# Performance work log

Measured on AMD Instinct MI355X. Metric: run time of the kernel, lower is better.

Reference implementation:

```python
import jax, jax.numpy as jnp
import numpy as np

NEG_INF = -1.0e9


def setup_inputs() -> dict:
    key = jax.random.key(0)
    ks = jax.random.split(key, 7)
    B, D, L, N, K = 4096, 512, 20, 8192, 64
    return {
        "inputs_embed": jax.random.normal(ks[0], (B, D), jnp.float32),
        "labels_embed": jax.random.normal(ks[1], (B, D), jnp.float32),
        "labels": jax.random.normal(ks[2], (B, L), jnp.float32),
        "all_labels_embed": jax.random.normal(ks[3], (N, D), jnp.float32),
        "all_labels": jax.random.normal(ks[4], (N, L), jnp.float32),
        "neg_ids_in": jax.random.randint(ks[5], (B, K), 0, B, jnp.int32),
        "neg_ids_lb": jax.random.randint(ks[6], (B, K), 0, N, jnp.int32),
    }


def reference(inputs_embed, labels_embed, labels, all_labels_embed, all_labels,
              neg_ids_in, neg_ids_lb):
    # --- negative sampling (indices supplied; equals tf.gather of tiled table) ---
    neg_ie = inputs_embed[neg_ids_in]        # [B,K,D] negatives from inputs
    neg_le = all_labels_embed[neg_ids_lb]    # [B,K,D] negatives from label table
    # bad-negative masks: negative label features identical to the positive's
    bad_in = jnp.all(labels[neg_ids_in] == labels[:, None, :], axis=-1).astype(inputs_embed.dtype)      # [B,K]
    bad_lb = jnp.all(all_labels[neg_ids_lb] == labels[:, None, :], axis=-1).astype(inputs_embed.dtype)  # [B,K]

    # --- similarities (dot products) ---
    sim_pos = jnp.sum(inputs_embed * labels_embed, axis=-1, keepdims=True)            # [B,1]
    sim_neg_il = jnp.einsum("bd,bkd->bk", inputs_embed, neg_le) + NEG_INF * bad_lb    # [B,K]
    sim_neg_ll = jnp.einsum("bd,bkd->bk", labels_embed, neg_le) + NEG_INF * bad_lb
    sim_neg_ii = jnp.einsum("bd,bkd->bk", inputs_embed, neg_ie) + NEG_INF * bad_in
    sim_neg_li = jnp.einsum("bd,bkd->bk", labels_embed, neg_ie) + NEG_INF * bad_in

    # --- accuracy ---
    max_all = jnp.max(jnp.concatenate([sim_pos, sim_neg_il], axis=-1), axis=-1)
    acc = jnp.mean((max_all == sim_pos[:, 0]).astype(jnp.float32))

    # --- softmax loss, correct class at index 0 ---
    logits = jnp.concatenate([sim_pos, sim_neg_il, sim_neg_ll, sim_neg_ii, sim_neg_li], axis=-1)  # [B,1+4K]
    per_ex = -jax.nn.log_softmax(logits, axis=-1)[:, 0]   # [B]

    # --- confidence-based loss scaling: loss_scale(-per_ex) ---
    q = jnp.exp(-per_ex)
    scale = jnp.where(jnp.max(q) > 0.5,
                      jax.lax.stop_gradient(((1.0 - q) / 0.5) ** 4),
                      jnp.ones_like(q))
    loss = jnp.mean(per_ex * scale)
    return loss, acc
```

## Files before the change

kernel.cpp:

```cpp
#include <hip/hip_runtime.h>
#include <hip/hip_bf16.h>

#define BB 4096
#define DD 512
#define LLAB 20
#define NN 8192
#define KK 64

constexpr float kNegInf = -1.0e9f;
constexpr float kLn2 = 0.69314718055994530942f;
constexpr float kWlPe = 2.5f;
constexpr float kWlTie = 2.0f;
constexpr double kFix = 1073741824.0;

#define OFF_PEREX 0
#define OFF_STATS 16384
#define OFF_MINPE (16384 + 256)
#define OFF_SUMP  (16384 + 512)
#define OFF_SUMS  (16384 + 1024)
#define OFF_SP    36864
#define OFF_SIE   53248
#define OFF_SLE   69632
#define OFF_SALE  86016
#define OFF_HLAB  118784
#define OFF_HAL   151552
#define OFF_IEQ   217088
#define OFF_LEQ   (OFF_IEQ + (size_t)BB * DD)
#define OFF_ALEQ  (OFF_LEQ + (size_t)BB * DD)
#define WS_NEED   (OFF_ALEQ + (size_t)NN * DD)

typedef unsigned u32x4 __attribute__((ext_vector_type(4)));

#define GLD(dst, base, OFFSTR)                                        \
  asm volatile("global_load_dwordx4 %0, %1, off offset:" OFFSTR      \
               : "=v"(dst) : "v"(base) : "memory")

__device__ __forceinline__ float dot4(const float4& a, const float4& b) {
  return a.x * b.x + a.y * b.y + a.z * b.z + a.w * b.w;
}

__device__ __forceinline__ float waveReduceSum(float v) {
#pragma unroll
  for (int s = 1; s < 64; s <<= 1) v += __shfl_xor(v, s);
  return v;
}

__device__ __forceinline__ float waveReduceMax(float v) {
#pragma unroll
  for (int s = 1; s < 64; s <<= 1) v = fmaxf(v, __shfl_xor(v, s));
  return v;
}

__device__ __forceinline__ float waveReduceMin(float v) {
#pragma unroll
  for (int s = 1; s < 64; s <<= 1) v = fminf(v, __shfl_xor(v, s));
  return v;
}

__device__ __forceinline__ unsigned long long hash20(const float* __restrict__ p) {
  unsigned long long h = 1469598103934665603ull;
#pragma unroll
  for (int t = 0; t < LLAB; ++t) {
    h ^= (unsigned long long)__float_as_uint(p[t]);
    h *= 1099511628211ull;
  }
  return h;
}

__device__ __forceinline__ int sdot4i(unsigned a, unsigned b, int acc) {
#if __has_builtin(__builtin_amdgcn_sdot4)
  return __builtin_amdgcn_sdot4((int)a, (int)b, acc, false);
#else
#pragma unroll
  for (int t = 0; t < 4; ++t)
    acc += (int)(signed char)(a >> (8 * t)) * (int)(signed char)(b >> (8 * t));
  return acc;
#endif
}

__device__ __forceinline__ unsigned pk4i8(float a, float b, float c, float d, float inv) {
  const int q0 = (int)rintf(a * inv);
  const int q1 = (int)rintf(b * inv);
  const int q2 = (int)rintf(c * inv);
  const int q3 = (int)rintf(d * inv);
  return (q0 & 255) | ((q1 & 255) << 8) | ((q2 & 255) << 16) | ((q3 & 255) << 24);
}

__device__ __forceinline__ float max8abs(const float4& a, const float4& c) {
  return fmaxf(fmaxf(fmaxf(fabsf(a.x), fabsf(a.y)), fmaxf(fabsf(a.z), fabsf(a.w))),
               fmaxf(fmaxf(fabsf(c.x), fabsf(c.y)), fmaxf(fabsf(c.z), fabsf(c.w))));
}

__device__ __forceinline__ float loss_scale(float pe) {
  const float q = expf(-pe);
  const float t = 2.0f * (1.0f - q);
  const float t2 = t * t;
  return t2 * t2;
}

__device__ __forceinline__ void accum_loss(int b, float pe, unsigned* minpeB,
                                           unsigned long long* sumP,
                                           unsigned long long* sumS) {
  const float pc = fmaxf(pe, 0.0f);
  const int bank = b & 63;
  atomicMin(&minpeB[bank], __float_as_uint(pc));
  atomicAdd(&sumP[bank], (unsigned long long)((double)pc * kFix + 0.5));
  atomicAdd(&sumS[bank],
            (unsigned long long)((double)(pc * loss_scale(pc)) * kFix + 0.5));
}

__global__ void init_kernel(unsigned* stats) {
  if (threadIdx.x == 0) stats[0] = 0u;
}

__global__ __launch_bounds__(256) void prep_kernel(
    const float* __restrict__ ie, const float* __restrict__ le,
    const float* __restrict__ ale, const float* __restrict__ labels,
    const float* __restrict__ al, char* __restrict__ ie_q,
    char* __restrict__ le_q, char* __restrict__ ale_q,
    float* __restrict__ s_ie, float* __restrict__ s_le,
    float* __restrict__ s_ale, float* __restrict__ sp,
    unsigned long long* __restrict__ h_lab,
    unsigned long long* __restrict__ h_al, unsigned* __restrict__ stats,
    unsigned* __restrict__ minpeB, unsigned long long* __restrict__ sumP,
    unsigned long long* __restrict__ sumS) {
  const int tid = threadIdx.x;
  const int lane = tid & 63;
  const int wave = tid >> 6;
  const int w = blockIdx.x * 4 + wave;

  if (w < BB) {
    const float4* i4 = (const float4*)(ie + (size_t)w * DD);
    const float4* l4 = (const float4*)(le + (size_t)w * DD);
    const float4 a0 = i4[2 * lane], a1 = i4[2 * lane + 1];
    const float4 b0 = l4[2 * lane], b1 = l4[2 * lane + 1];
    float p = dot4(a0, b0) + dot4(a1, b1);
    p = waveReduceSum(p);
    float mi = fmaxf(waveReduceMax(max8abs(a0, a1)), 1e-20f);
    const float inv_i = 127.0f / mi;
    uint2 oi;
    oi.x = pk4i8(a0.x, a0.y, a0.z, a0.w, inv_i);
    oi.y = pk4i8(a1.x, a1.y, a1.z, a1.w, inv_i);
    ((uint2*)(ie_q + (size_t)w * DD))[lane] = oi;
    float ml = fmaxf(waveReduceMax(max8abs(b0, b1)), 1e-20f);
    const float inv_l = 127.0f / ml;
    uint2 ol;
    ol.x = pk4i8(b0.x, b0.y, b0.z, b0.w, inv_l);
    ol.y = pk4i8(b1.x, b1.y, b1.z, b1.w, inv_l);
    ((uint2*)(le_q + (size_t)w * DD))[lane] = ol;
    if (lane == 0) {
      sp[w] = p;
      s_ie[w] = mi * (1.0f / 127.0f);
      s_le[w] = ml * (1.0f / 127.0f);
    }
  } else {
    const int row = w - BB;
    const float4* r4 = (const float4*)(ale + (size_t)row * DD);
    const float4 a = r4[2 * lane], c = r4[2 * lane + 1];
    float mx = fmaxf(waveReduceMax(max8abs(a, c)), 1e-20f);
    const float inv = 127.0f / mx;
    uint2 o;
    o.x = pk4i8(a.x, a.y, a.z, a.w, inv);
    o.y = pk4i8(c.x, c.y, c.z, c.w, inv);
    ((uint2*)(ale_q + (size_t)row * DD))[lane] = o;
    if (lane == 0) s_ale[row] = mx * (1.0f / 127.0f);
  }

  const int g = blockIdx.x * 256 + tid;
  if (g < 2) stats[g] = 0u;
  if (g < 64) {
    minpeB[g] = 0x7F800000u;
    sumP[g] = 0ull;
    sumS[g] = 0ull;
  }
  if (g < BB) h_lab[g] = hash20(labels + (size_t)g * LLAB);
  else if (g < BB + NN) h_al[g - BB] = hash20(al + (size_t)(g - BB) * LLAB);
}

__device__ __forceinline__ void row_f32_body(
    int b, const float* __restrict__ ie, const float* __restrict__ le,
    const float* __restrict__ labels, const float* __restrict__ ale,
    const float* __restrict__ al, const int* __restrict__ nin,
    const int* __restrict__ nlb, float* __restrict__ per_ex,
    unsigned* __restrict__ stats, bool count_acc, float* sims, float* wred) {
  const int tid = threadIdx.x;
  const int lane = tid & 63;
  const int wave = tid >> 6;

  const float4* ie4 = (const float4*)(ie + (size_t)b * DD);
  const float4* le4 = (const float4*)(le + (size_t)b * DD);
  float4 ier0 = ie4[lane], ier1 = ie4[lane + 64];
  float4 ler0 = le4[lane], ler1 = le4[lane + 64];
  float lab = (lane < LLAB) ? labels[(size_t)b * LLAB + lane] : 0.0f;

  if (wave == 0) {
    float p = dot4(ier0, ler0) + dot4(ier1, ler1);
    p = waveReduceSum(p);
    if (lane == 0) sims[0] = p;
  }

#pragma unroll 2
  for (int kk = 0; kk < KK / 4; ++kk) {
    const int k = wave * (KK / 4) + kk;
    const int j_lb = __builtin_amdgcn_readfirstlane(nlb[(size_t)b * KK + k]);
    const int j_in = __builtin_amdgcn_readfirstlane(nin[(size_t)b * KK + k]);

    const float4* rle = (const float4*)(ale + (size_t)j_lb * DD);
    const float4* rie = (const float4*)(ie + (size_t)j_in * DD);
    float4 vle0 = rle[lane], vle1 = rle[lane + 64];
    float4 vie0 = rie[lane], vie1 = rie[lane + 64];

    bool ein = true, elb = true;
    if (lane < LLAB) {
      ein = (labels[(size_t)j_in * LLAB + lane] == lab);
      elb = (al[(size_t)j_lb * LLAB + lane] == lab);
    }
    const bool bad_in = (__ballot(ein) == ~0ull);
    const bool bad_lb = (__ballot(elb) == ~0ull);

    float a_il = dot4(vle0, ier0) + dot4(vle1, ier1);
    float a_ll = dot4(vle0, ler0) + dot4(vle1, ler1);
    float a_ii = dot4(vie0, ier0) + dot4(vie1, ier1);
    float a_li = dot4(vie0, ler0) + dot4(vie1, ler1);

    const bool oddl = (lane & 1) != 0;
    float sx = oddl ? a_il : a_ii;
    float sy = oddl ? a_ll : a_li;
    float rx = __shfl_xor(sx, 1);
    float ry = __shfl_xor(sy, 1);
    float mx = (oddl ? a_ii : a_il) + rx;
    float my = (oddl ? a_li : a_ll) + ry;
    const bool hi2 = (lane & 2) != 0;
    float s1 = hi2 ? mx : my;
    float r1 = __shfl_xor(s1, 2);
    float v = (hi2 ? my : mx) + r1;
    v += __shfl_xor(v, 4);
    v += __shfl_xor(v, 8);
    v += __shfl_xor(v, 16);
    v += __shfl_xor(v, 32);

    if (lane < 4) {
      const bool badf = (lane & 1) ? bad_in : bad_lb;
      const float s = badf ? v + kNegInf : v;
      const int slot = ((lane & 1) << 1) | ((lane >> 1) & 1);
      sims[1 + slot * KK + k] = s;
    }
  }
  __syncthreads();

  const float v = sims[1 + tid];
  const float s0 = sims[0];
  float wmax = waveReduceMax(v);
  if (lane == 0) wred[wave] = wmax;
  __syncthreads();
  float m = fmaxf(fmaxf(wred[0], wred[1]), fmaxf(wred[2], wred[3]));
  m = fmaxf(m, s0);
  const float e = expf(v - m);
  float wsum = waveReduceSum(e);
  if (lane == 0) wred[4 + wave] = wsum;
  __syncthreads();
  if (tid == 0) {
    const float tot = wred[4] + wred[5] + wred[6] + wred[7] + expf(s0 - m);
    per_ex[b] = m + logf(tot) - s0;
    if (count_acc) {
      const float max_il = wred[0];
      if (s0 >= max_il) atomicAdd(&stats[0], 1u);
    }
  }
}

__global__ __launch_bounds__(256, 4) void row_i8_kernel(
    const float* __restrict__ ie, const float* __restrict__ le,
    const float* __restrict__ labels, const float* __restrict__ ale,
    const float* __restrict__ al, const char* __restrict__ ie_q,
    const char* __restrict__ le_q, const char* __restrict__ ale_q,
    const float* __restrict__ s_ie, const float* __restrict__ s_le,
    const float* __restrict__ s_ale, const float* __restrict__ sp,
    const unsigned long long* __restrict__ h_lab,
    const unsigned long long* __restrict__ h_al,
    const int* __restrict__ nin, const int* __restrict__ nlb,
    float* __restrict__ per_ex, unsigned* __restrict__ stats,
    unsigned* __restrict__ minpeB, unsigned long long* __restrict__ sumP,
    unsigned long long* __restrict__ sumS) {
  const int b = blockIdx.x;
  const int tid = threadIdx.x;
  const int lane = tid & 63;
  const int wave = tid >> 6;
  const int c = lane & 3;
  const int g = lane >> 2;

  __shared__ u32x4 qls4[64];
  __shared__ float simsX[1 + 4 * KK];
  __shared__ float wred[12];
  __shared__ int do_fix;

  {
    const u32x4* qsrc = (lane < 32)
        ? ((const u32x4*)(ie_q + ((size_t)b << 9))) + lane
        : ((const u32x4*)(le_q + ((size_t)b << 9))) + (lane - 32);
    qls4[lane] = *qsrc;
  }

  const int wuni = __builtin_amdgcn_readfirstlane(wave);
  const int k = wuni * 16 + g;
  const int jl = nlb[b * KK + k];
  const int ji = nin[b * KK + k];
  const char* pa = ale_q + ((size_t)jl << 9) + (c << 4);
  const char* pb = ie_q + ((size_t)ji << 9) + (c << 4);

  u32x4 A0, A1, A2, A3, A4, A5, A6, A7;
  u32x4 B0, B1, B2, B3, B4, B5, B6, B7;
  GLD(A0, pa, "0");   GLD(A1, pa, "64");  GLD(A2, pa, "128"); GLD(A3, pa, "192");
  GLD(A4, pa, "256"); GLD(A5, pa, "320"); GLD(A6, pa, "384"); GLD(A7, pa, "448");
  GLD(B0, pb, "0");   GLD(B1, pb, "64");  GLD(B2, pb, "128"); GLD(B3, pb, "192");
  GLD(B4, pb, "256"); GLD(B5, pb, "320"); GLD(B6, pb, "384"); GLD(B7, pb, "448");

  const unsigned long long hb = h_lab[b];
  const bool bad_lb = (h_al[jl] == hb);
  const bool bad_in = (h_lab[ji] == hb);
  const float sA = s_ale[jl];
  const float sB = s_ie[ji];
  const float s0 = sp[b];
  const float sqi = s_ie[b];
  const float sql = s_le[b];

  asm volatile("s_waitcnt vmcnt(0)" ::: "memory");
  __builtin_amdgcn_sched_barrier(0);

  int il = 0, ll = 0, ii = 0, li = 0;
#define STEP(Ai, Bi, i)                                              \
  {                                                                  \
    const u32x4 qi = qls4[(i) * 4 + c];                              \
    const u32x4 ql = qls4[32 + (i) * 4 + c];                         \
    il = sdot4i(Ai.x, qi.x, il); il = sdot4i(Ai.y, qi.y, il);        \
    il = sdot4i(Ai.z, qi.z, il); il = sdot4i(Ai.w, qi.w, il);        \
    ll = sdot4i(Ai.x, ql.x, ll); ll = sdot4i(Ai.y, ql.y, ll);        \
    ll = sdot4i(Ai.z, ql.z, ll); ll = sdot4i(Ai.w, ql.w, ll);        \
    ii = sdot4i(Bi.x, qi.x, ii); ii = sdot4i(Bi.y, qi.y, ii);        \
    ii = sdot4i(Bi.z, qi.z, ii); ii = sdot4i(Bi.w, qi.w, ii);        \
    li = sdot4i(Bi.x, ql.x, li); li = sdot4i(Bi.y, ql.y, li);        \
    li = sdot4i(Bi.z, ql.z, li); li = sdot4i(Bi.w, ql.w, li);        \
  }
  STEP(A0, B0, 0) STEP(A1, B1, 1) STEP(A2, B2, 2) STEP(A3, B3, 3)
  STEP(A4, B4, 4) STEP(A5, B5, 5) STEP(A6, B6, 6) STEP(A7, B7, 7)
#undef STEP

  const bool odd = (lane & 1) != 0;
  const int x = odd ? il : ii;
  const int y = odd ? ll : li;
  const int rx = __shfl_xor(x, 1);
  const int ry = __shfl_xor(y, 1);
  const int aa = (odd ? ii : il) + rx;
  const int bb2 = (odd ? li : ll) + ry;
  const bool hi2 = (lane & 2) != 0;
  const int s1 = hi2 ? aa : bb2;
  const int r1 = __shfl_xor(s1, 2);
  const int vi = (hi2 ? bb2 : aa) + r1;

  const float srow = (c & 1) ? sB : sA;
  const float sq = (c & 2) ? sql : sqi;
  const float v = (float)vi * (srow * sq);
  const bool badf = (c & 1) ? bad_in : bad_lb;
  const float s = badf ? v + kNegInf : v;

  float m_w = waveReduceMax(s);
  float mil_w = waveReduceMax((c == 0) ? s : -3.0e38f);
  if (lane == 0) {
    wred[wave] = m_w;
    wred[4 + wave] = mil_w;
  }
  __syncthreads();
  float m = fmaxf(fmaxf(fmaxf(wred[0], wred[1]), fmaxf(wred[2], wred[3])), s0);
  const float e = expf(s - m);
  float sum_w = waveReduceSum(e);
  if (lane == 0) wred[8 + wave] = sum_w;
  __syncthreads();
  if (tid == 0) {
    const float tot =
        wred[8] + wred[9] + wred[10] + wred[11] + expf(s0 - m);
    const float pe = m + logf(tot) - s0;
    per_ex[b] = pe;
    const float max_il = fmaxf(fmaxf(wred[4], wred[5]), fmaxf(wred[6], wred[7]));
    const bool wl_row = (pe < kWlPe) || (fabsf(s0 - max_il) < kWlTie);
    do_fix = wl_row ? 1 : 0;
    if (!wl_row) {
      if (s0 >= max_il) atomicAdd(&stats[0], 1u);
      accum_loss(b, pe, minpeB, sumP, sumS);
    }
  }
  __syncthreads();

  if (do_fix) {
    row_f32_body(b, ie, le, labels, ale, al, nin, nlb, per_ex, stats,
                 true, simsX, wred);
    if (tid == 0) accum_loss(b, per_ex[b], minpeB, sumP, sumS);
  }
}

__global__ __launch_bounds__(256) void row_f32_kernel(
    const float* __restrict__ ie, const float* __restrict__ le,
    const float* __restrict__ labels, const float* __restrict__ ale,
    const float* __restrict__ al, const int* __restrict__ nin,
    const int* __restrict__ nlb, float* __restrict__ per_ex,
    unsigned* __restrict__ stats) {
  __shared__ float sims[1 + 4 * KK];
  __shared__ float wred[8];
  row_f32_body(blockIdx.x, ie, le, labels, ale, al, nin, nlb, per_ex, stats,
               true, sims, wred);
}

__global__ __launch_bounds__(64) void finalize2_kernel(
    const unsigned* __restrict__ stats, const unsigned* __restrict__ minpeB,
    const unsigned long long* __restrict__ sumP,
    const unsigned long long* __restrict__ sumS, float* __restrict__ out) {
  const int lane = threadIdx.x;
  unsigned mb = minpeB[lane];
  unsigned long long p = sumP[lane];
  unsigned long long q = sumS[lane];
#pragma unroll
  for (int s = 1; s < 64; s <<= 1) {
    mb = min(mb, (unsigned)__shfl_xor((int)mb, s));
    p += (unsigned long long)__shfl_xor((long long)p, s);
    q += (unsigned long long)__shfl_xor((long long)q, s);
  }
  if (lane == 0) {
    const float minpe = __uint_as_float(mb);
    const bool scale_on = (minpe < kLn2);
    const double tot = (double)(scale_on ? q : p) / kFix;
    out[0] = (float)(tot / (double)BB);
    out[1] = (float)stats[0] / (float)BB;
  }
}

__global__ __launch_bounds__(256) void finalize_kernel(
    const float* __restrict__ per_ex, const unsigned* __restrict__ stats,
    float* __restrict__ out) {
  __shared__ float pe_s[BB];
  __shared__ float wred[8];
  const int tid = threadIdx.x;
  const int lane = tid & 63;
  const int wave = tid >> 6;

  float mn = 1.0e30f;
#pragma unroll 4
  for (int i = tid; i < BB; i += 256) {
    const float v = per_ex[i];
    pe_s[i] = v;
    mn = fminf(mn, v);
  }
  mn = waveReduceMin(mn);
  if (lane == 0) wred[wave] = mn;
  __syncthreads();
  const float minpe = fminf(fminf(wred[0], wred[1]), fminf(wred[2], wred[3]));
  const bool scale_on = (minpe < kLn2);
  __syncthreads();

  float sum = 0.0f;
#pragma unroll 4
  for (int i = tid; i < BB; i += 256) {
    const float pe = pe_s[i];
    sum += pe * (scale_on ? loss_scale(pe) : 1.0f);
  }
  sum = waveReduceSum(sum);
  if (lane == 0) wred[4 + wave] = sum;
  __syncthreads();
  if (tid == 0) {
    const float tot = wred[4] + wred[5] + wred[6] + wred[7];
    out[0] = tot / (float)BB;
    out[1] = (float)stats[0] / (float)BB;
  }
}

extern "C" void kernel_launch(void* const* d_in, const int* in_sizes, int n_in,
                              void* d_out, int out_size, void* d_ws, size_t ws_size,
                              hipStream_t stream) {
  const float* ie = (const float*)d_in[0];
  const float* le = (const float*)d_in[1];
  const float* labels = (const float*)d_in[2];
  const float* ale = (const float*)d_in[3];
  const float* al = (const float*)d_in[4];
  const int* nin = (const int*)d_in[5];
  const int* nlb = (const int*)d_in[6];
  float* out = (float*)d_out;

  float* per_ex = (float*)d_ws;
  unsigned* stats = (unsigned*)((char*)d_ws + OFF_STATS);

  if (ws_size >= WS_NEED) {
    char* ie_q = (char*)d_ws + OFF_IEQ;
    char* le_q = (char*)d_ws + OFF_LEQ;
    char* ale_q = (char*)d_ws + OFF_ALEQ;
    float* s_ie = (float*)((char*)d_ws + OFF_SIE);
    float* s_le = (float*)((char*)d_ws + OFF_SLE);
    float* s_ale = (float*)((char*)d_ws + OFF_SALE);
    float* sp = (float*)((char*)d_ws + OFF_SP);
    unsigned long long* h_lab = (unsigned long long*)((char*)d_ws + OFF_HLAB);
    unsigned long long* h_al = (unsigned long long*)((char*)d_ws + OFF_HAL);
    unsigned* minpeB = (unsigned*)((char*)d_ws + OFF_MINPE);
    unsigned long long* sumP = (unsigned long long*)((char*)d_ws + OFF_SUMP);
    unsigned long long* sumS = (unsigned long long*)((char*)d_ws + OFF_SUMS);

    const int prep_blocks = (BB + NN) / 4;
    hipLaunchKernelGGL(prep_kernel, dim3(prep_blocks), dim3(256), 0, stream,
                       ie, le, ale, labels, al, ie_q, le_q, ale_q,
                       s_ie, s_le, s_ale, sp, h_lab, h_al, stats,
                       minpeB, sumP, sumS);
    hipLaunchKernelGGL(row_i8_kernel, dim3(BB), dim3(256), 0, stream,
                       ie, le, labels, ale, al, ie_q, le_q, ale_q,
                       s_ie, s_le, s_ale, sp, h_lab, h_al, nin, nlb,
                       per_ex, stats, minpeB, sumP, sumS);
    hipLaunchKernelGGL(finalize2_kernel, dim3(1), dim3(64), 0, stream,
                       stats, minpeB, sumP, sumS, out);
  } else {
    hipLaunchKernelGGL(init_kernel, dim3(1), dim3(64), 0, stream, stats);
    hipLaunchKernelGGL(row_f32_kernel, dim3(BB), dim3(256), 0, stream,
                       ie, le, labels, ale, al, nin, nlb, per_ex, stats);
    hipLaunchKernelGGL(finalize_kernel, dim3(1), dim3(256), 0, stream,
                       per_ex, stats, out);
  }
}
```

Baseline: 53.63 us.

## Process four rows per block with double-buffered gather loads overlapping compute

The int8 row kernel now handles four batch rows per block, launching a quarter as many blocks. It preloads indices, scales and bad-negative flags into shared memory, with the bad flag encoded as the sign of the scale. Gathered negatives are fetched in two register sets so the loads for the next half-row overlap the dot products of the current one. The aim is to hide gather latency and amortise per-block setup, at the cost of fewer blocks, more registers and serialised per-row softmax barriers.

```diff
diff --git a/kernel.cpp b/kernel.cpp
--- a/kernel.cpp
+++ b/kernel.cpp
@@ -34,6 +34,16 @@
 #define GLD(dst, base, OFFSTR)                                        \
   asm volatile("global_load_dwordx4 %0, %1, off offset:" OFFSTR      \
                : "=v"(dst) : "v"(base) : "memory")
+
+#define VWAIT8 do { asm volatile("s_waitcnt vmcnt(8)" ::: "memory"); \
+                    __builtin_amdgcn_sched_barrier(0); } while (0)
+#define VWAIT0 do { asm volatile("s_waitcnt vmcnt(0)" ::: "memory"); \
+                    __builtin_amdgcn_sched_barrier(0); } while (0)
+
+#define LBAR do { __builtin_amdgcn_sched_barrier(0);                  \
+                  asm volatile("s_waitcnt lgkmcnt(0)" ::: "memory");  \
+                  __builtin_amdgcn_s_barrier();                       \
+                  __builtin_amdgcn_sched_barrier(0); } while (0)
 
 __device__ __forceinline__ float dot4(const float4& a, const float4& b) {
   return a.x * b.x + a.y * b.y + a.z * b.z + a.w * b.w;
@@ -269,7 +279,7 @@
   }
 }
 
-__global__ __launch_bounds__(256, 4) void row_i8_kernel(
+__global__ __launch_bounds__(256) void row_i8_kernel(
     const float* __restrict__ ie, const float* __restrict__ le,
     const float* __restrict__ labels, const float* __restrict__ ale,
     const float* __restrict__ al, const char* __restrict__ ie_q,
@@ -282,119 +292,186 @@
     float* __restrict__ per_ex, unsigned* __restrict__ stats,
     unsigned* __restrict__ minpeB, unsigned long long* __restrict__ sumP,
     unsigned long long* __restrict__ sumS) {
-  const int b = blockIdx.x;
+  const int b0 = blockIdx.x * 4;
   const int tid = threadIdx.x;
   const int lane = tid & 63;
   const int wave = tid >> 6;
-  const int c = lane & 3;
-  const int g = lane >> 2;
-
-  __shared__ u32x4 qls4[64];
-  __shared__ float simsX[1 + 4 * KK];
-  __shared__ float wred[12];
+  const int o = lane & 7;
+  const int oct = lane >> 3;
+
+  __shared__ u32x4 qls[256];
+  __shared__ int jls[256], jis[256];
+  __shared__ float sAs[256], sBs[256];
+  __shared__ float sims[1 + 4 * KK];
+  __shared__ float wred[8];
   __shared__ int do_fix;
 
   {
+    const int r = wave;
+    const int br = b0 + r;
     const u32x4* qsrc = (lane < 32)
-        ? ((const u32x4*)(ie_q + ((size_t)b << 9))) + lane
-        : ((const u32x4*)(le_q + ((size_t)b << 9))) + (lane - 32);
-    qls4[lane] = *qsrc;
-  }
-
-  const int wuni = __builtin_amdgcn_readfirstlane(wave);
-  const int k = wuni * 16 + g;
-  const int jl = nlb[b * KK + k];
-  const int ji = nin[b * KK + k];
-  const char* pa = ale_q + ((size_t)jl << 9) + (c << 4);
-  const char* pb = ie_q + ((size_t)ji << 9) + (c << 4);
+        ? ((const u32x4*)(ie_q + ((size_t)br << 9))) + lane
+        : ((const u32x4*)(le_q + ((size_t)br << 9))) + (lane - 32);
+    qls[r * 64 + lane] = *qsrc;
+
+    const int k = tid & 63;
+    const int jl = nlb[br * KK + k];
+    const int ji = nin[br * KK + k];
+    const unsigned long long hbr = h_lab[br];
+    const bool blb = (h_al[jl] == hbr);
+    const bool bin = (h_lab[ji] == hbr);
+    const float sa = s_ale[jl];
+    const float sb = s_ie[ji];
+    jls[tid] = jl;
+    jis[tid] = ji;
+    sAs[tid] = blb ? -sa : sa;
+    sBs[tid] = bin ? -sb : sb;
+  }
+  float sp_r[4], sqi_r[4], sql_r[4];
+#pragma unroll
+  for (int rr = 0; rr < 4; ++rr) {
+    sp_r[rr] = sp[b0 + rr];
+    sqi_r[rr] = s_ie[b0 + rr];
+    sql_r[rr] = s_le[b0 + rr];
+  }
+  __syncthreads();
 
   u32x4 A0, A1, A2, A3, A4, A5, A6, A7;
   u32x4 B0, B1, B2, B3, B4, B5, B6, B7;
-  GLD(A0, pa, "0");   GLD(A1, pa, "64");  GLD(A2, pa, "128"); GLD(A3, pa, "192");
-  GLD(A4, pa, "256"); GLD(A5, pa, "320"); GLD(A6, pa, "384"); GLD(A7, pa, "448");
-  GLD(B0, pb, "0");   GLD(B1, pb, "64");  GLD(B2, pb, "128"); GLD(B3, pb, "192");
-  GLD(B4, pb, "256"); GLD(B5, pb, "320"); GLD(B6, pb, "384"); GLD(B7, pb, "448");
-
-  const unsigned long long hb = h_lab[b];
-  const bool bad_lb = (h_al[jl] == hb);
-  const bool bad_in = (h_lab[ji] == hb);
-  const float sA = s_ale[jl];
-  const float sB = s_ie[ji];
-  const float s0 = sp[b];
-  const float sqi = s_ie[b];
-  const float sql = s_le[b];
-
-  asm volatile("s_waitcnt vmcnt(0)" ::: "memory");
-  __builtin_amdgcn_sched_barrier(0);
-
-  int il = 0, ll = 0, ii = 0, li = 0;
-#define STEP(Ai, Bi, i)                                              \
-  {                                                                  \
-    const u32x4 qi = qls4[(i) * 4 + c];                              \
-    const u32x4 ql = qls4[32 + (i) * 4 + c];                         \
-    il = sdot4i(Ai.x, qi.x, il); il = sdot4i(Ai.y, qi.y, il);        \
-    il = sdot4i(Ai.z, qi.z, il); il = sdot4i(Ai.w, qi.w, il);        \
-    ll = sdot4i(Ai.x, ql.x, ll); ll = sdot4i(Ai.y, ql.y, ll);        \
-    ll = sdot4i(Ai.z, ql.z, ll); ll = sdot4i(Ai.w, ql.w, ll);        \
-    ii = sdot4i(Bi.x, qi.x, ii); ii = sdot4i(Bi.y, qi.y, ii);        \
-    ii = sdot4i(Bi.z, qi.z, ii); ii = sdot4i(Bi.w, qi.w, ii);        \
-    li = sdot4i(Bi.x, ql.x, li); li = sdot4i(Bi.y, ql.y, li);        \
-    li = sdot4i(Bi.z, ql.z, li); li = sdot4i(Bi.w, ql.w, li);        \
-  }
-  STEP(A0, B0, 0) STEP(A1, B1, 1) STEP(A2, B2, 2) STEP(A3, B3, 3)
-  STEP(A4, B4, 4) STEP(A5, B5, 5) STEP(A6, B6, 6) STEP(A7, B7, 7)
-#undef STEP
-
-  const bool odd = (lane & 1) != 0;
-  const int x = odd ? il : ii;
-  const int y = odd ? ll : li;
-  const int rx = __shfl_xor(x, 1);
-  const int ry = __shfl_xor(y, 1);
-  const int aa = (odd ? ii : il) + rx;
-  const int bb2 = (odd ? li : ll) + ry;
-  const bool hi2 = (lane & 2) != 0;
-  const int s1 = hi2 ? aa : bb2;
-  const int r1 = __shfl_xor(s1, 2);
-  const int vi = (hi2 ? bb2 : aa) + r1;
-
-  const float srow = (c & 1) ? sB : sA;
-  const float sq = (c & 2) ? sql : sqi;
-  const float v = (float)vi * (srow * sq);
-  const bool badf = (c & 1) ? bad_in : bad_lb;
-  const float s = badf ? v + kNegInf : v;
-
-  float m_w = waveReduceMax(s);
-  float mil_w = waveReduceMax((c == 0) ? s : -3.0e38f);
-  if (lane == 0) {
-    wred[wave] = m_w;
-    wred[4 + wave] = mil_w;
-  }
-  __syncthreads();
-  float m = fmaxf(fmaxf(fmaxf(wred[0], wred[1]), fmaxf(wred[2], wred[3])), s0);
-  const float e = expf(s - m);
-  float sum_w = waveReduceSum(e);
-  if (lane == 0) wred[8 + wave] = sum_w;
-  __syncthreads();
-  if (tid == 0) {
-    const float tot =
-        wred[8] + wred[9] + wred[10] + wred[11] + expf(s0 - m);
-    const float pe = m + logf(tot) - s0;
-    per_ex[b] = pe;
-    const float max_il = fmaxf(fmaxf(wred[4], wred[5]), fmaxf(wred[6], wred[7]));
-    const bool wl_row = (pe < kWlPe) || (fabsf(s0 - max_il) < kWlTie);
-    do_fix = wl_row ? 1 : 0;
-    if (!wl_row) {
-      if (s0 >= max_il) atomicAdd(&stats[0], 1u);
-      accum_loss(b, pe, minpeB, sumP, sumS);
-    }
-  }
-  __syncthreads();
-
-  if (do_fix) {
-    row_f32_body(b, ie, le, labels, ale, al, nin, nlb, per_ex, stats,
-                 true, simsX, wred);
-    if (tid == 0) accum_loss(b, per_ex[b], minpeB, sumP, sumS);
-  }
+
+#define ISSUE8(S, rr, hh)                                                 \
+  {                                                                       \
+    const int k_ = (hh) * 32 + (wave << 3) + oct;                         \
+    const int jl_ = jls[(rr) * 64 + k_];                                  \
+    const int ji_ = jis[(rr) * 64 + k_];                                  \
+    const char* pa_ = ale_q + ((size_t)jl_ << 9) + (o << 4);              \
+    const char* pb_ = ie_q + ((size_t)ji_ << 9) + (o << 4);               \
+    GLD(S##0, pa_, "0");   GLD(S##1, pa_, "128");                         \
+    GLD(S##2, pa_, "256"); GLD(S##3, pa_, "384");                         \
+    GLD(S##4, pb_, "0");   GLD(S##5, pb_, "128");                         \
+    GLD(S##6, pb_, "256"); GLD(S##7, pb_, "384");                         \
+  }
+
+#define COMPUTE8(S, rr, hh)                                               \
+  {                                                                       \
+    const u32x4 a0_ = S##0, a1_ = S##1, a2_ = S##2, a3_ = S##3;           \
+    const u32x4 e0_ = S##4, e1_ = S##5, e2_ = S##6, e3_ = S##7;           \
+    const int k_ = (hh) * 32 + (wave << 3) + oct;                         \
+    const u32x4 q0 = qls[(rr) * 64 + o];                                  \
+    const u32x4 q1 = qls[(rr) * 64 + o + 8];                              \
+    const u32x4 q2 = qls[(rr) * 64 + o + 16];                             \
+    const u32x4 q3 = qls[(rr) * 64 + o + 24];                             \
+    const u32x4 l0 = qls[(rr) * 64 + 32 + o];                             \
+    const u32x4 l1 = qls[(rr) * 64 + 32 + o + 8];                         \
+    const u32x4 l2 = qls[(rr) * 64 + 32 + o + 16];                        \
+    const u32x4 l3 = qls[(rr) * 64 + 32 + o + 24];                        \
+    int il = 0, ll = 0, ii = 0, li = 0;                                   \
+    il = sdot4i(a0_.x, q0.x, il); il = sdot4i(a0_.y, q0.y, il);           \
+    il = sdot4i(a0_.z, q0.z, il); il = sdot4i(a0_.w, q0.w, il);           \
+    il = sdot4i(a1_.x, q1.x, il); il = sdot4i(a1_.y, q1.y, il);           \
+    il = sdot4i(a1_.z, q1.z, il); il = sdot4i(a1_.w, q1.w, il);           \
+    il = sdot4i(a2_.x, q2.x, il); il = sdot4i(a2_.y, q2.y, il);           \
+    il = sdot4i(a2_.z, q2.z, il); il = sdot4i(a2_.w, q2.w, il);           \
+    il = sdot4i(a3_.x, q3.x, il); il = sdot4i(a3_.y, q3.y, il);           \
+    il = sdot4i(a3_.z, q3.z, il); il = sdot4i(a3_.w, q3.w, il);           \
+    ll = sdot4i(a0_.x, l0.x, ll); ll = sdot4i(a0_.y, l0.y, ll);           \
+    ll = sdot4i(a0_.z, l0.z, ll); ll = sdot4i(a0_.w, l0.w, ll);           \
+    ll = sdot4i(a1_.x, l1.x, ll); ll = sdot4i(a1_.y, l1.y, ll);           \
+    ll = sdot4i(a1_.z, l1.z, ll); ll = sdot4i(a1_.w, l1.w, ll);           \
+    ll = sdot4i(a2_.x, l2.x, ll); ll = sdot4i(a2_.y, l2.y, ll);           \
+    ll = sdot4i(a2_.z, l2.z, ll); ll = sdot4i(a2_.w, l2.w, ll);           \
+    ll = sdot4i(a3_.x, l3.x, ll); ll = sdot4i(a3_.y, l3.y, ll);           \
+    ll = sdot4i(a3_.z, l3.z, ll); ll = sdot4i(a3_.w, l3.w, ll);           \
+    ii = sdot4i(e0_.x, q0.x, ii); ii = sdot4i(e0_.y, q0.y, ii);           \
+    ii = sdot4i(e0_.z, q0.z, ii); ii = sdot4i(e0_.w, q0.w, ii);           \
+    ii = sdot4i(e1_.x, q1.x, ii); ii = sdot4i(e1_.y, q1.y, ii);           \
+    ii = sdot4i(e1_.z, q1.z, ii); ii = sdot4i(e1_.w, q1.w, ii);           \
+    ii = sdot4i(e2_.x, q2.x, ii); ii = sdot4i(e2_.y, q2.y, ii);           \
+    ii = sdot4i(e2_.z, q2.z, ii); ii = sdot4i(e2_.w, q2.w, ii);           \
+    ii = sdot4i(e3_.x, q3.x, ii); ii = sdot4i(e3_.y, q3.y, ii);           \
+    ii = sdot4i(e3_.z, q3.z, ii); ii = sdot4i(e3_.w, q3.w, ii);           \
+    li = sdot4i(e0_.x, l0.x, li); li = sdot4i(e0_.y, l0.y, li);           \
+    li = sdot4i(e0_.z, l0.z, li); li = sdot4i(e0_.w, l0.w, li);           \
+    li = sdot4i(e1_.x, l1.x, li); li = sdot4i(e1_.y, l1.y, li);           \
+    li = sdot4i(e1_.z, l1.z, li); li = sdot4i(e1_.w, l1.w, li);           \
+    li = sdot4i(e2_.x, l2.x, li); li = sdot4i(e2_.y, l2.y, li);           \
+    li = sdot4i(e2_.z, l2.z, li); li = sdot4i(e2_.w, l2.w, li);           \
+    li = sdot4i(e3_.x, l3.x, li); li = sdot4i(e3_.y, l3.y, li);           \
+    li = sdot4i(e3_.z, l3.z, li); li = sdot4i(e3_.w, l3.w, li);           \
+    const bool odd = (lane & 1) != 0;                                     \
+    const int x_ = odd ? il : ii;                                         \
+    const int y_ = odd ? ll : li;                                         \
+    const int rx_ = __shfl_xor(x_, 1);                                    \
+    const int ry_ = __shfl_xor(y_, 1);                                    \
+    const int aa_ = (odd ? ii : il) + rx_;                                \
+    const int bb_ = (odd ? li : ll) + ry_;                                \
+    const bool hi2_ = (lane & 2) != 0;                                    \
+    const int s1_ = hi2_ ? aa_ : bb_;                                     \
+    const int r1_ = __shfl_xor(s1_, 2);                                   \
+    int vi_ = (hi2_ ? bb_ : aa_) + r1_;                                   \
+    vi_ += __shfl_xor(vi_, 4);                                            \
+    if ((lane & 4) == 0) {                                                \
+      const int c_ = lane & 3;                                            \
+      const float scq = (c_ & 1) ? sBs[(rr) * 64 + k_]                    \
+                                 : sAs[(rr) * 64 + k_];                   \
+      const float sq_ = (c_ & 2) ? sql_r[rr] : sqi_r[rr];                 \
+      float v_ = (float)vi_ * (fabsf(scq) * sq_);                         \
+      if (scq < 0.0f) v_ += kNegInf;                                      \
+      const int slot_ = ((c_ & 1) << 1) | (c_ >> 1);                      \
+      sims[1 + slot_ * KK + k_] = v_;                                     \
+    }                                                                     \
+  }
+
+#define LSE(rr)                                                           \
+  {                                                                       \
+    LBAR;                                                                 \
+    const float vv = sims[1 + tid];                                       \
+    const float s0 = sp_r[rr];                                            \
+    float wmax = waveReduceMax(vv);                                       \
+    if (lane == 0) wred[wave] = wmax;                                     \
+    LBAR;                                                                 \
+    float m = fmaxf(fmaxf(wred[0], wred[1]), fmaxf(wred[2], wred[3]));    \
+    m = fmaxf(m, s0);                                                     \
+    const float e = expf(vv - m);                                         \
+    float wsum = waveReduceSum(e);                                        \
+    if (lane == 0) wred[4 + wave] = wsum;                                 \
+    LBAR;                                                                 \
+    if (tid == 0) {                                                       \
+      const float tot = wred[4] + wred[5] + wred[6] + wred[7] +           \
+                        expf(s0 - m);                                     \
+      const float pe = m + logf(tot) - s0;                                \
+      per_ex[b0 + (rr)] = pe;                                             \
+      const float max_il = wred[0];                                       \
+      const bool wl_row = (pe < kWlPe) || (fabsf(s0 - max_il) < kWlTie);  \
+      do_fix = wl_row ? 1 : 0;                                            \
+      if (!wl_row) {                                                      \
+        if (s0 >= max_il) atomicAdd(&stats[0], 1u);                       \
+        accum_loss(b0 + (rr), pe, minpeB, sumP, sumS);                    \
+      }                                                                   \
+    }                                                                     \
+    LBAR;                                                                 \
+    if (do_fix) {                                                         \
+      row_f32_body(b0 + (rr), ie, le, labels, ale, al, nin, nlb,          \
+                   per_ex, stats, true, sims, wred);                      \
+      if (tid == 0) accum_loss(b0 + (rr), per_ex[b0 + (rr)],              \
+                               minpeB, sumP, sumS);                       \
+      __syncthreads();                                                    \
+    }                                                                     \
+  }
+
+  ISSUE8(A, 0, 0);
+  ISSUE8(B, 0, 1); VWAIT8; COMPUTE8(A, 0, 0);
+  ISSUE8(A, 1, 0); VWAIT8; COMPUTE8(B, 0, 1); LSE(0);
+  ISSUE8(B, 1, 1); VWAIT8; COMPUTE8(A, 1, 0);
+  ISSUE8(A, 2, 0); VWAIT8; COMPUTE8(B, 1, 1); LSE(1);
+  ISSUE8(B, 2, 1); VWAIT8; COMPUTE8(A, 2, 0);
+  ISSUE8(A, 3, 0); VWAIT8; COMPUTE8(B, 2, 1); LSE(2);
+  ISSUE8(B, 3, 1); VWAIT8; COMPUTE8(A, 3, 0);
+                   VWAIT0; COMPUTE8(B, 3, 1); LSE(3);
+
+#undef ISSUE8
+#undef COMPUTE8
+#undef LSE
 }
 
 __global__ __launch_bounds__(256) void row_f32_kernel(
@@ -505,7 +582,7 @@
                        ie, le, ale, labels, al, ie_q, le_q, ale_q,
                        s_ie, s_le, s_ale, sp, h_lab, h_al, stats,
                        minpeB, sumP, sumS);
-    hipLaunchKernelGGL(row_i8_kernel, dim3(BB), dim3(256), 0, stream,
+    hipLaunchKernelGGL(row_i8_kernel, dim3(BB / 4), dim3(256), 0, stream,
                        ie, le, labels, ale, al, ie_q, le_q, ale_q,
                        s_ie, s_le, s_ale, sp, h_lab, h_al, nin, nlb,
                        per_ex, stats, minpeB, sumP, sumS);
```

Result: slower. 60.49 us (+12.8%).

## Split int8 row kernel into two gather passes staged through workspace

Applied to the files above, without the earlier changes.

Replaces the single row kernel, which gathered both the label-table and input negatives at once, with two kernels. Pass A gathers the all_labels_embed negatives and writes 128 sims per row to workspace. Pass B gathers the input negatives, reads those sims back, and does the softmax and fixup. The aim is a smaller per-pass working set (ale_q vs ie_q) for better cache locality and fewer registers, allowing higher occupancy. The cost is an extra launch and a global round trip of the sims.

```diff
diff --git a/kernel.cpp b/kernel.cpp
--- a/kernel.cpp
+++ b/kernel.cpp
@@ -27,13 +27,17 @@
 #define OFF_IEQ   217088
 #define OFF_LEQ   (OFF_IEQ + (size_t)BB * DD)
 #define OFF_ALEQ  (OFF_LEQ + (size_t)BB * DD)
-#define WS_NEED   (OFF_ALEQ + (size_t)NN * DD)
+#define OFF_SIMS  (OFF_ALEQ + (size_t)NN * DD)
+#define WS_NEED   (OFF_SIMS + (size_t)BB * 128 * 4)
 
 typedef unsigned u32x4 __attribute__((ext_vector_type(4)));
 
 #define GLD(dst, base, OFFSTR)                                        \
   asm volatile("global_load_dwordx4 %0, %1, off offset:" OFFSTR      \
                : "=v"(dst) : "v"(base) : "memory")
+
+#define VWAIT0 do { asm volatile("s_waitcnt vmcnt(0)" ::: "memory"); \
+                    __builtin_amdgcn_sched_barrier(0); } while (0)
 
 __device__ __forceinline__ float dot4(const float4& a, const float4& b) {
   return a.x * b.x + a.y * b.y + a.z * b.z + a.w * b.w;
@@ -177,6 +181,83 @@
   else if (g < BB + NN) h_al[g - BB] = hash20(al + (size_t)(g - BB) * LLAB);
 }
 
+__device__ __forceinline__ void gather2dots(const char* __restrict__ tab_q,
+                                            int j, int c,
+                                            const u32x4* __restrict__ qls4,
+                                            int& outA, int& outB, int lane) {
+  const char* base = tab_q + ((size_t)j << 9) + (c << 4);
+  u32x4 T0, T1, T2, T3, T4, T5, T6, T7;
+  GLD(T0, base, "0");   GLD(T1, base, "64");
+  GLD(T2, base, "128"); GLD(T3, base, "192");
+  GLD(T4, base, "256"); GLD(T5, base, "320");
+  GLD(T6, base, "384"); GLD(T7, base, "448");
+  VWAIT0;
+  int dA = 0, dB = 0;
+#define DOTI(T, i)                                                    \
+  {                                                                   \
+    const u32x4 qi = qls4[(i) * 4 + c];                               \
+    const u32x4 ql = qls4[32 + (i) * 4 + c];                          \
+    dA = sdot4i(T.x, qi.x, dA); dA = sdot4i(T.y, qi.y, dA);           \
+    dA = sdot4i(T.z, qi.z, dA); dA = sdot4i(T.w, qi.w, dA);           \
+    dB = sdot4i(T.x, ql.x, dB); dB = sdot4i(T.y, ql.y, dB);           \
+    dB = sdot4i(T.z, ql.z, dB); dB = sdot4i(T.w, ql.w, dB);           \
+  }
+  DOTI(T0, 0) DOTI(T1, 1) DOTI(T2, 2) DOTI(T3, 3)
+  DOTI(T4, 4) DOTI(T5, 5) DOTI(T6, 6) DOTI(T7, 7)
+#undef DOTI
+  const bool odd = (lane & 1) != 0;
+  const int keep = odd ? dB : dA;
+  const int send = odd ? dA : dB;
+  const int r = __shfl_xor(send, 1);
+  int val = keep + r;
+  val += __shfl_xor(val, 2);
+  outA = val;
+  outB = val;
+}
+
+__global__ __launch_bounds__(256, 8) void passa_kernel(
+    const char* __restrict__ ale_q, const float* __restrict__ s_ale,
+    const unsigned long long* __restrict__ h_al,
+    const char* __restrict__ ie_q, const char* __restrict__ le_q,
+    const float* __restrict__ s_ie, const float* __restrict__ s_le,
+    const unsigned long long* __restrict__ h_lab,
+    const int* __restrict__ nlb, float* __restrict__ sims_ws) {
+  const int b = blockIdx.x;
+  const int tid = threadIdx.x;
+  const int lane = tid & 63;
+  const int wave = tid >> 6;
+  const int c = lane & 3;
+  const int g = lane >> 2;
+
+  __shared__ u32x4 qls4[64];
+  {
+    const u32x4* qsrc = (lane < 32)
+        ? ((const u32x4*)(ie_q + ((size_t)b << 9))) + lane
+        : ((const u32x4*)(le_q + ((size_t)b << 9))) + (lane - 32);
+    qls4[lane] = *qsrc;
+  }
+
+  const int k = wave * 16 + g;
+  const int j = nlb[b * KK + k];
+  const bool bad = (h_al[j] == h_lab[b]);
+  const float st = s_ale[j];
+  const float sqi = s_ie[b];
+  const float sql = s_le[b];
+
+  int vA, vB;
+  gather2dots(ale_q, j, c, qls4, vA, vB, lane);
+
+  if (c == 0) {
+    float v = (float)vA * (st * sqi);
+    if (bad) v += kNegInf;
+    sims_ws[(size_t)b * 128 + k] = v;
+  } else if (c == 1) {
+    float v = (float)vB * (st * sql);
+    if (bad) v += kNegInf;
+    sims_ws[(size_t)b * 128 + 64 + k] = v;
+  }
+}
+
 __device__ __forceinline__ void row_f32_body(
     int b, const float* __restrict__ ie, const float* __restrict__ le,
     const float* __restrict__ labels, const float* __restrict__ ale,
@@ -269,18 +350,17 @@
   }
 }
 
-__global__ __launch_bounds__(256, 4) void row_i8_kernel(
+__global__ __launch_bounds__(256, 6) void passb_kernel(
     const float* __restrict__ ie, const float* __restrict__ le,
     const float* __restrict__ labels, const float* __restrict__ ale,
     const float* __restrict__ al, const char* __restrict__ ie_q,
-    const char* __restrict__ le_q, const char* __restrict__ ale_q,
-    const float* __restrict__ s_ie, const float* __restrict__ s_le,
-    const float* __restrict__ s_ale, const float* __restrict__ sp,
+    const char* __restrict__ le_q, const float* __restrict__ s_ie,
+    const float* __restrict__ s_le, const float* __restrict__ sp,
     const unsigned long long* __restrict__ h_lab,
-    const unsigned long long* __restrict__ h_al,
     const int* __restrict__ nin, const int* __restrict__ nlb,
-    float* __restrict__ per_ex, unsigned* __restrict__ stats,
-    unsigned* __restrict__ minpeB, unsigned long long* __restrict__ sumP,
+    const float* __restrict__ sims_ws, float* __restrict__ per_ex,
+    unsigned* __restrict__ stats, unsigned* __restrict__ minpeB,
+    unsigned long long* __restrict__ sumP,
     unsigned long long* __restrict__ sumS) {
   const int b = blockIdx.x;
   const int tid = threadIdx.x;
@@ -291,7 +371,7 @@
 
   __shared__ u32x4 qls4[64];
   __shared__ float simsX[1 + 4 * KK];
-  __shared__ float wred[12];
+  __shared__ float wred[8];
   __shared__ int do_fix;
 
   {
@@ -301,86 +381,47 @@
     qls4[lane] = *qsrc;
   }
 
-  const int wuni = __builtin_amdgcn_readfirstlane(wave);
-  const int k = wuni * 16 + g;
-  const int jl = nlb[b * KK + k];
-  const int ji = nin[b * KK + k];
-  const char* pa = ale_q + ((size_t)jl << 9) + (c << 4);
-  const char* pb = ie_q + ((size_t)ji << 9) + (c << 4);
-
-  u32x4 A0, A1, A2, A3, A4, A5, A6, A7;
-  u32x4 B0, B1, B2, B3, B4, B5, B6, B7;
-  GLD(A0, pa, "0");   GLD(A1, pa, "64");  GLD(A2, pa, "128"); GLD(A3, pa, "192");
-  GLD(A4, pa, "256"); GLD(A5, pa, "320"); GLD(A6, pa, "384"); GLD(A7, pa, "448");
-  GLD(B0, pb, "0");   GLD(B1, pb, "64");  GLD(B2, pb, "128"); GLD(B3, pb, "192");
-  GLD(B4, pb, "256"); GLD(B5, pb, "320"); GLD(B6, pb, "384"); GLD(B7, pb, "448");
-
-  const unsigned long long hb = h_lab[b];
-  const bool bad_lb = (h_al[jl] == hb);
-  const bool bad_in = (h_lab[ji] == hb);
-  const float sA = s_ale[jl];
-  const float sB = s_ie[ji];
-  const float s0 = sp[b];
+  const int k = wave * 16 + g;
+  const int j = nin[b * KK + k];
+  const bool bad = (h_lab[j] == h_lab[b]);
+  const float st = s_ie[j];
   const float sqi = s_ie[b];
   const float sql = s_le[b];
 
-  asm volatile("s_waitcnt vmcnt(0)" ::: "memory");
-  __builtin_amdgcn_sched_barrier(0);
-
-  int il = 0, ll = 0, ii = 0, li = 0;
-#define STEP(Ai, Bi, i)                                              \
-  {                                                                  \
-    const u32x4 qi = qls4[(i) * 4 + c];                              \
-    const u32x4 ql = qls4[32 + (i) * 4 + c];                         \
-    il = sdot4i(Ai.x, qi.x, il); il = sdot4i(Ai.y, qi.y, il);        \
-    il = sdot4i(Ai.z, qi.z, il); il = sdot4i(Ai.w, qi.w, il);        \
-    ll = sdot4i(Ai.x, ql.x, ll); ll = sdot4i(Ai.y, ql.y, ll);        \
-    ll = sdot4i(Ai.z, ql.z, ll); ll = sdot4i(Ai.w, ql.w, ll);        \
-    ii = sdot4i(Bi.x, qi.x, ii); ii = sdot4i(Bi.y, qi.y, ii);        \
-    ii = sdot4i(Bi.z, qi.z, ii); ii = sdot4i(Bi.w, qi.w, ii);        \
-    li = sdot4i(Bi.x, ql.x, li); li = sdot4i(Bi.y, ql.y, li);        \
-    li = sdot4i(Bi.z, ql.z, li); li = sdot4i(Bi.w, ql.w, li);        \
-  }
-  STEP(A0, B0, 0) STEP(A1, B1, 1) STEP(A2, B2, 2) STEP(A3, B3, 3)
-  STEP(A4, B4, 4) STEP(A5, B5, 5) STEP(A6, B6, 6) STEP(A7, B7, 7)
-#undef STEP
-
-  const bool odd = (lane & 1) != 0;
-  const int x = odd ? il : ii;
-  const int y = odd ? ll : li;
-  const int rx = __shfl_xor(x, 1);
-  const int ry = __shfl_xor(y, 1);
-  const int aa = (odd ? ii : il) + rx;
-  const int bb2 = (odd ? li : ll) + ry;
-  const bool hi2 = (lane & 2) != 0;
-  const int s1 = hi2 ? aa : bb2;
-  const int r1 = __shfl_xor(s1, 2);
-  const int vi = (hi2 ? bb2 : aa) + r1;
-
-  const float srow = (c & 1) ? sB : sA;
-  const float sq = (c & 2) ? sql : sqi;
-  const float v = (float)vi * (srow * sq);
-  const bool badf = (c & 1) ? bad_in : bad_lb;
-  const float s = badf ? v + kNegInf : v;
-
-  float m_w = waveReduceMax(s);
-  float mil_w = waveReduceMax((c == 0) ? s : -3.0e38f);
-  if (lane == 0) {
-    wred[wave] = m_w;
-    wred[4 + wave] = mil_w;
-  }
-  __syncthreads();
-  float m = fmaxf(fmaxf(fmaxf(wred[0], wred[1]), fmaxf(wred[2], wred[3])), s0);
-  const float e = expf(s - m);
-  float sum_w = waveReduceSum(e);
-  if (lane == 0) wred[8 + wave] = sum_w;
+  int vA, vB;
+  gather2dots(ie_q, j, c, qls4, vA, vB, lane);
+
+  if (c == 0) {
+    float v = (float)vA * (st * sqi);
+    if (bad) v += kNegInf;
+    simsX[1 + 128 + k] = v;
+  } else if (c == 1) {
+    float v = (float)vB * (st * sql);
+    if (bad) v += kNegInf;
+    simsX[1 + 192 + k] = v;
+  }
+  __syncthreads();
+
+  if (tid < 128) simsX[1 + tid] = sims_ws[(size_t)b * 128 + tid];
+  if (tid == 0) simsX[0] = sp[b];
+  __syncthreads();
+
+  const float v = simsX[1 + tid];
+  const float s0 = simsX[0];
+  float wmax = waveReduceMax(v);
+  if (lane == 0) wred[wave] = wmax;
+  __syncthreads();
+  float m = fmaxf(fmaxf(wred[0], wred[1]), fmaxf(wred[2], wred[3]));
+  m = fmaxf(m, s0);
+  const float e = expf(v - m);
+  float wsum = waveReduceSum(e);
+  if (lane == 0) wred[4 + wave] = wsum;
   __syncthreads();
   if (tid == 0) {
-    const float tot =
-        wred[8] + wred[9] + wred[10] + wred[11] + expf(s0 - m);
+    const float tot = wred[4] + wred[5] + wred[6] + wred[7] + expf(s0 - m);
     const float pe = m + logf(tot) - s0;
     per_ex[b] = pe;
-    const float max_il = fmaxf(fmaxf(wred[4], wred[5]), fmaxf(wred[6], wred[7]));
+    const float max_il = wred[0];
     const bool wl_row = (pe < kWlPe) || (fabsf(s0 - max_il) < kWlTie);
     do_fix = wl_row ? 1 : 0;
     if (!wl_row) {
@@ -499,16 +540,20 @@
     unsigned* minpeB = (unsigned*)((char*)d_ws + OFF_MINPE);
     unsigned long long* sumP = (unsigned long long*)((char*)d_ws + OFF_SUMP);
     unsigned long long* sumS = (unsigned long long*)((char*)d_ws + OFF_SUMS);
+    float* sims_ws = (float*)((char*)d_ws + OFF_SIMS);
 
     const int prep_blocks = (BB + NN) / 4;
     hipLaunchKernelGGL(prep_kernel, dim3(prep_blocks), dim3(256), 0, stream,
                        ie, le, ale, labels, al, ie_q, le_q, ale_q,
                        s_ie, s_le, s_ale, sp, h_lab, h_al, stats,
                        minpeB, sumP, sumS);
-    hipLaunchKernelGGL(row_i8_kernel, dim3(BB), dim3(256), 0, stream,
-                       ie, le, labels, ale, al, ie_q, le_q, ale_q,
-                       s_ie, s_le, s_ale, sp, h_lab, h_al, nin, nlb,
-                       per_ex, stats, minpeB, sumP, sumS);
+    hipLaunchKernelGGL(passa_kernel, dim3(BB), dim3(256), 0, stream,
+                       ale_q, s_ale, h_al, ie_q, le_q, s_ie, s_le, h_lab,
+                       nlb, sims_ws);
+    hipLaunchKernelGGL(passb_kernel, dim3(BB), dim3(256), 0, stream,
+                       ie, le, labels, ale, al, ie_q, le_q, s_ie, s_le, sp,
+                       h_lab, nin, nlb, sims_ws, per_ex, stats,
+                       minpeB, sumP, sumS);
     hipLaunchKernelGGL(finalize2_kernel, dim3(1), dim3(64), 0, stream,
                        stats, minpeB, sumP, sumS, out);
   } else {
```

Result: slower. 65.38 us (+21.9%).
